# Performance work log

Hardware: AMD Instinct MI355X
Metric: run time of the kernel (lower is better)

Reference implementation:

```python
import jax, jax.numpy as jnp
import numpy as np

B, C, L = 32, 512, 4096
H, K = 8, 3            # heads, kernel_size
D = C // H             # head dim
G = 32                 # GroupNorm groups
PAD = (K - 1) // 2
EPS = 1e-5
NEG = -1e30


def setup_inputs() -> dict:
    key = jax.random.key(0)
    ks = jax.random.split(key, 7)
    s = 0.02
    return {
        "x": jax.random.normal(ks[0], (B, C, L), dtype=jnp.float32),
        "gamma": jnp.ones((C,), dtype=jnp.float32),
        "beta": jnp.zeros((C,), dtype=jnp.float32),
        "W_k": jax.random.normal(ks[1], (C, H * D), dtype=jnp.float32) * s,
        "W_v": jax.random.normal(ks[2], (C, H * D), dtype=jnp.float32) * s,
        "W_o": jax.random.normal(ks[3], (H * D, C), dtype=jnp.float32) * s,
        "q": jax.random.normal(ks[4], (H, D), dtype=jnp.float32) * s,     # learned queries (QnA)
        "rpe": jax.random.normal(ks[5], (H, K), dtype=jnp.float32) * s,   # relative-position bias
    }


def _group_norm(x, gamma, beta):
    # x: (B, C, L); normalize over (C//G, L) within each of G groups
    b, c, l = x.shape
    xg = x.reshape(b, G, (c // G) * l)
    mu = jnp.mean(xg, axis=-1, keepdims=True)
    var = jnp.var(xg, axis=-1, keepdims=True)
    xn = ((xg - mu) * jax.lax.rsqrt(var + EPS)).reshape(b, c, l)
    return xn * gamma[None, :, None] + beta[None, :, None]


def reference(x, gamma, beta, W_k, W_v, W_o, q, rpe):
    h = _group_norm(x, gamma, beta)                     # (B, C, L)
    ht = jnp.transpose(h, (0, 2, 1))                    # (B, L, C)
    k = (ht @ W_k).reshape(B, L, H, D)                  # (B, L, H, D)
    v = (ht @ W_v).reshape(B, L, H, D)

    scale = 1.0 / np.sqrt(D).astype(np.float32)
    logits = jnp.einsum('blhd,hd->blh', k, q) * scale   # (B, L, H)

    # sliding windows of size K (zero-padded; -inf logits at boundaries)
    lp = jnp.pad(logits, ((0, 0), (PAD, PAD), (0, 0)), constant_values=NEG)
    lwin = jnp.stack([lp[:, j:j + L] for j in range(K)], axis=2)      # (B, L, K, H)
    lwin = lwin + jnp.transpose(rpe)[None, None]                       # rpe: (H,K)->(K,H)
    attn = jax.nn.softmax(lwin, axis=2)                                # (B, L, K, H)

    vp = jnp.pad(v, ((0, 0), (PAD, PAD), (0, 0), (0, 0)))
    vwin = jnp.stack([vp[:, j:j + L] for j in range(K)], axis=2)       # (B, L, K, H, D)
    o = jnp.einsum('blkh,blkhd->blhd', attn, vwin).reshape(B, L, H * D)

    out = (o @ W_o)                                      # (B, L, C)
    return x + jnp.transpose(out, (0, 2, 1))             # residual, (B, C, L)
```

## Files before the change

kernel.cpp:

```cpp
#include <hip/hip_runtime.h>

#define Bb 32
#define Cc 512
#define Ll 4096
#define Hh 8
#define Dd 64
#define Gg 32
#define BLt (Bb * Ll)
#define NKV 520
#define NKVPAD 640

typedef __attribute__((ext_vector_type(4))) float f32x4;
typedef __attribute__((ext_vector_type(8))) short short8;
typedef __attribute__((ext_vector_type(4))) int int4v;

union U16 { int4v v; short s[8]; };

__device__ __forceinline__ float bf2f(short s) {
    unsigned u = ((unsigned)(unsigned short)s) << 16;
    float f; __builtin_memcpy(&f, &u, 4); return f;
}
__device__ __forceinline__ short f2bf(float f) {
    unsigned u; __builtin_memcpy(&u, &f, 4);
    u = (u + 0x7FFFu + ((u >> 16) & 1u)) >> 16;
    return (short)u;
}

__device__ __forceinline__ int swz_off(int row, int inner) {
    return row * 128 + (inner ^ ((row & 7) << 4));
}

__global__ void k_prep(const float* __restrict__ Wk, const float* __restrict__ Wv,
                       const float* __restrict__ Wo, const float* __restrict__ q,
                       short* __restrict__ Wct, short* __restrict__ Wot)
{
    int bid = blockIdx.x, t = threadIdx.x;
    if (bid < NKVPAD) {
        int n = bid;
        if (n < 512) {
            for (int k = t; k < 512; k += 64)
                Wct[n * 512 + k] = f2bf(Wv[k * 512 + n]);
        } else if (n < NKV) {
            int h = n - 512;
            for (int k = t; k < 512; k += 64) {
                float acc = 0.f;
                for (int d = 0; d < 64; ++d)
                    acc += Wk[k * 512 + h * 64 + d] * q[h * 64 + d];
                Wct[n * 512 + k] = f2bf(acc * 0.125f);
            }
        } else {
            for (int k = t; k < 512; k += 64) Wct[n * 512 + k] = 0;
        }
    } else {
        int c = bid - NKVPAD;
        for (int k = t; k < 512; k += 64)
            Wot[c * 512 + k] = f2bf(Wo[k * 512 + c]);
    }
}

__global__ void k_stats(const float* __restrict__ x, float* __restrict__ stats)
{
    int bg = blockIdx.x;
    const float* p = x + (size_t)bg * 65536;
    int t = threadIdx.x;
    float s = 0.f, ss = 0.f;
    for (int i = t * 4; i < 65536; i += 1024) {
        f32x4 v = *(const f32x4*)(p + i);
        s  += v[0] + v[1] + v[2] + v[3];
        ss += v[0]*v[0] + v[1]*v[1] + v[2]*v[2] + v[3]*v[3];
    }
    for (int o = 32; o > 0; o >>= 1) { s += __shfl_down(s, o); ss += __shfl_down(ss, o); }
    __shared__ float red[8];
    int lane = t & 63, w = t >> 6;
    if (lane == 0) { red[w] = s; red[4 + w] = ss; }
    __syncthreads();
    if (t == 0) {
        float S  = red[0] + red[1] + red[2] + red[3];
        float SS = red[4] + red[5] + red[6] + red[7];
        float mean = S * (1.0f / 65536.0f);
        float var  = SS * (1.0f / 65536.0f) - mean * mean;
        stats[bg * 2]     = mean;
        stats[bg * 2 + 1] = rsqrtf(var + 1e-5f);
    }
}

__global__ void k_norm_t(const float* __restrict__ x, const float* __restrict__ gamma,
                         const float* __restrict__ beta, const float* __restrict__ stats,
                         short* __restrict__ hT)
{
    __shared__ float tile[64 * 65];
    int b = blockIdx.z, c0 = blockIdx.y * 64, l0 = blockIdx.x * 64;
    int t = threadIdx.x;
    int lq = t & 15, cq = t >> 4;
    #pragma unroll
    for (int p = 0; p < 4; ++p) {
        int cl = cq + p * 16;
        int c = c0 + cl;
        float mean = stats[(b * 32 + (c >> 4)) * 2];
        float rstd = stats[(b * 32 + (c >> 4)) * 2 + 1];
        float a  = rstd * gamma[c];
        float bb = beta[c] - mean * a;
        f32x4 v = *(const f32x4*)(x + ((size_t)b << 21) + ((size_t)c << 12) + l0 + lq * 4);
        #pragma unroll
        for (int j = 0; j < 4; ++j) tile[cl * 65 + lq * 4 + j] = v[j] * a + bb;
    }
    __syncthreads();
    int ll = t >> 2, cq4 = t & 3;
    int bl = b * Ll + l0 + ll;
    short hbuf[16];
    #pragma unroll
    for (int j = 0; j < 16; ++j) hbuf[j] = f2bf(tile[(cq4 * 16 + j) * 65 + ll]);
    short8* dst = (short8*)(hT + (size_t)bl * 512 + c0 + cq4 * 16);
    dst[0] = *(short8*)&hbuf[0];
    dst[1] = *(short8*)&hbuf[8];
}

__launch_bounds__(256, 2)
__global__ void k_gemm1(const short* __restrict__ hT, const short* __restrict__ Wct,
                        short* __restrict__ kv)
{
    __shared__ short sA[2][8192];
    __shared__ short sB[2][8192];
    const int t = threadIdx.x;
    const int m0 = blockIdx.y * 128;
    const int n0 = blockIdx.x * 128;
    const int lane = t & 63, wid = t >> 6;
    const int wm = wid >> 1, wn = wid & 1;
    const int g = lane >> 4, ln = lane & 15;
    const int sr = t >> 1, ksh = t & 1;

    const short* gA = hT  + (size_t)(m0 + sr) * 512 + ksh * 32;
    const short* gB = Wct + (size_t)(n0 + sr) * 512 + ksh * 32;

    f32x4 acc[4][4] = {};
    U16 ra[4], rb[4];

    auto load_tile = [&](int kt) {
        #pragma unroll
        for (int q = 0; q < 4; ++q) {
            ra[q].v = *(const int4v*)(gA + kt * 64 + q * 8);
            rb[q].v = *(const int4v*)(gB + kt * 64 + q * 8);
        }
    };
    auto write_tile = [&](int buf) {
        #pragma unroll
        for (int f = 0; f < 4; ++f) {
            U16 wa, wb;
            #pragma unroll
            for (int j = 0; j < 4; ++j) {
                wa.s[j]     = ra[f >> 1].s[(f & 1) * 4 + j];
                wa.s[4 + j] = ra[2 + (f >> 1)].s[(f & 1) * 4 + j];
                wb.s[j]     = rb[f >> 1].s[(f & 1) * 4 + j];
                wb.s[4 + j] = rb[2 + (f >> 1)].s[(f & 1) * 4 + j];
            }
            int off = swz_off(sr, ksh * 64 + f * 16);
            *(int4v*)((char*)&sA[buf][0] + off) = wa.v;
            *(int4v*)((char*)&sB[buf][0] + off) = wb.v;
        }
    };
    auto compute = [&](int buf) {
        #pragma unroll
        for (int ks = 0; ks < 2; ++ks) {
            short8 af[4], bfr[4];
            #pragma unroll
            for (int i = 0; i < 4; ++i) {
                af[i]  = *(const short8*)((const char*)&sA[buf][0] + swz_off(wm * 64 + i * 16 + ln, ks * 64 + g * 16));
                bfr[i] = *(const short8*)((const char*)&sB[buf][0] + swz_off(wn * 64 + i * 16 + ln, ks * 64 + g * 16));
            }
            #pragma unroll
            for (int mi = 0; mi < 4; ++mi)
                #pragma unroll
                for (int ni = 0; ni < 4; ++ni)
                    acc[mi][ni] = __builtin_amdgcn_mfma_f32_16x16x32_bf16(af[mi], bfr[ni], acc[mi][ni], 0, 0, 0);
        }
    };

    load_tile(0); write_tile(0); __syncthreads();
    #pragma unroll 1
    for (int kt = 0; kt < 8; ++kt) {
        if (kt < 7) load_tile(kt + 1);
        compute(kt & 1);
        if (kt < 7) write_tile((kt + 1) & 1);
        __syncthreads();
    }

    #pragma unroll
    for (int mi = 0; mi < 4; ++mi)
        #pragma unroll
        for (int ni = 0; ni < 4; ++ni)
            #pragma unroll
            for (int i = 0; i < 4; ++i) {
                int m = m0 + wm * 64 + mi * 16 + g * 4 + i;
                int n = n0 + wn * 64 + ni * 16 + ln;
                if (n < NKV) kv[(size_t)m * NKV + n] = f2bf(acc[mi][ni][i]);
            }
}

__global__ void k_attnw(const short* __restrict__ kv, const float* __restrict__ rpe,
                        float* __restrict__ attnW)
{
    int tid = blockIdx.x * 256 + threadIdx.x;
    int bl = tid >> 3, h = tid & 7;
    int l = bl & (Ll - 1);
    float lg[3];
    #pragma unroll
    for (int j = 0; j < 3; ++j) {
        bool valid = (j == 1) || (j == 0 && l > 0) || (j == 2 && l < Ll - 1);
        lg[j] = valid ? (bf2f(kv[(size_t)(bl + j - 1) * NKV + 512 + h]) + rpe[h * 3 + j])
                      : -1e30f;
    }
    float m = fmaxf(lg[0], fmaxf(lg[1], lg[2]));
    float e0 = __expf(lg[0] - m), e1 = __expf(lg[1] - m), e2 = __expf(lg[2] - m);
    float inv = 1.0f / (e0 + e1 + e2);
    f32x4 w = { e0 * inv, e1 * inv, e2 * inv, 0.0f };
    *(f32x4*)(attnW + (size_t)bl * 32 + h * 4) = w;
}

__launch_bounds__(256, 2)
__global__ void k_gemm2(const short* __restrict__ Wot, const short* __restrict__ kv,
                        const float* __restrict__ attnW, const float* __restrict__ x,
                        float* __restrict__ out)
{
    __shared__ short sA[2][8192];
    __shared__ short sB[2][8192];
    const int t = threadIdx.x;
    const int m0 = blockIdx.x * 128;
    const int n0 = blockIdx.y * 128;
    const int lane = t & 63, wid = t >> 6;
    const int wm = wid >> 1, wn = wid & 1;
    const int g = lane >> 4, ln = lane & 15;
    const int sr = t >> 1, ksh = t & 1;

    const short* gA = Wot + (size_t)(m0 + sr) * 512 + ksh * 32;
    const int nrow = n0 + sr;
    const int lpos = nrow & (Ll - 1);
    const int nm1 = (lpos == 0) ? nrow : nrow - 1;
    const int np1 = (lpos == Ll - 1) ? nrow : nrow + 1;
    const short* gV0 = kv + (size_t)nrow * NKV + ksh * 32;
    const short* gVm = kv + (size_t)nm1  * NKV + ksh * 32;
    const short* gVp = kv + (size_t)np1  * NKV + ksh * 32;
    const float* gW = attnW + (size_t)nrow * 32;

    f32x4 acc[4][4] = {};
    U16 ra[4], rbm[4], rb0[4], rbp[4];
    f32x4 wv;

    auto load_tile = [&](int kt) {
        #pragma unroll
        for (int q = 0; q < 4; ++q) {
            ra[q].v  = *(const int4v*)(gA  + kt * 64 + q * 8);
            rbm[q].v = *(const int4v*)(gVm + kt * 64 + q * 8);
            rb0[q].v = *(const int4v*)(gV0 + kt * 64 + q * 8);
            rbp[q].v = *(const int4v*)(gVp + kt * 64 + q * 8);
        }
        wv = *(const f32x4*)(gW + kt * 4);
    };
    auto write_tile = [&](int buf) {
        short ob[32];
        #pragma unroll
        for (int q = 0; q < 4; ++q)
            #pragma unroll
            for (int j = 0; j < 8; ++j) {
                float o = wv[0] * bf2f(rbm[q].s[j]) + wv[1] * bf2f(rb0[q].s[j])
                        + wv[2] * bf2f(rbp[q].s[j]);
                ob[q * 8 + j] = f2bf(o);
            }
        #pragma unroll
        for (int f = 0; f < 4; ++f) {
            U16 wa, wb;
            #pragma unroll
            for (int j = 0; j < 4; ++j) {
                wa.s[j]     = ra[f >> 1].s[(f & 1) * 4 + j];
                wa.s[4 + j] = ra[2 + (f >> 1)].s[(f & 1) * 4 + j];
                wb.s[j]     = ob[4 * f + j];
                wb.s[4 + j] = ob[16 + 4 * f + j];
            }
            int off = swz_off(sr, ksh * 64 + f * 16);
            *(int4v*)((char*)&sA[buf][0] + off) = wa.v;
            *(int4v*)((char*)&sB[buf][0] + off) = wb.v;
        }
    };
    auto compute = [&](int buf) {
        #pragma unroll
        for (int ks = 0; ks < 2; ++ks) {
            short8 af[4], bfr[4];
            #pragma unroll
            for (int i = 0; i < 4; ++i) {
                af[i]  = *(const short8*)((const char*)&sA[buf][0] + swz_off(wm * 64 + i * 16 + ln, ks * 64 + g * 16));
                bfr[i] = *(const short8*)((const char*)&sB[buf][0] + swz_off(wn * 64 + i * 16 + ln, ks * 64 + g * 16));
            }
            #pragma unroll
            for (int mi = 0; mi < 4; ++mi)
                #pragma unroll
                for (int ni = 0; ni < 4; ++ni)
                    acc[mi][ni] = __builtin_amdgcn_mfma_f32_16x16x32_bf16(af[mi], bfr[ni], acc[mi][ni], 0, 0, 0);
        }
    };

    load_tile(0); write_tile(0); __syncthreads();
    #pragma unroll 1
    for (int kt = 0; kt < 8; ++kt) {
        if (kt < 7) load_tile(kt + 1);
        compute(kt & 1);
        if (kt < 7) write_tile((kt + 1) & 1);
        __syncthreads();
    }

    #pragma unroll
    for (int mi = 0; mi < 4; ++mi)
        #pragma unroll
        for (int ni = 0; ni < 4; ++ni)
            #pragma unroll
            for (int i = 0; i < 4; ++i) {
                int c = m0 + wm * 64 + mi * 16 + g * 4 + i;
                int ng = n0 + wn * 64 + ni * 16 + ln;
                int b = ng >> 12, l = ng & (Ll - 1);
                size_t off = ((size_t)b << 21) | ((size_t)c << 12) | (size_t)l;
                out[off] = x[off] + acc[mi][ni][i];
            }
}

extern "C" void kernel_launch(void* const* d_in, const int* in_sizes, int n_in,
                              void* d_out, int out_size, void* d_ws, size_t ws_size,
                              hipStream_t stream)
{
    const float* x     = (const float*)d_in[0];
    const float* gamma = (const float*)d_in[1];
    const float* beta  = (const float*)d_in[2];
    const float* Wk    = (const float*)d_in[3];
    const float* Wv    = (const float*)d_in[4];
    const float* Wo    = (const float*)d_in[5];
    const float* q     = (const float*)d_in[6];
    const float* rpe   = (const float*)d_in[7];
    float* out = (float*)d_out;

    char* ws = (char*)d_ws;
    short* Wct   = (short*)(ws + 0);
    short* Wot   = (short*)(ws + 655360);
    float* stats = (float*)(ws + 1179648);
    float* attnW = (float*)(ws + 1187840);
    short* kv    = (short*)(ws + 17965056);
    short* hT    = (short*)d_out;

    k_prep<<<1152, 64, 0, stream>>>(Wk, Wv, Wo, q, Wct, Wot);
    k_stats<<<1024, 256, 0, stream>>>(x, stats);
    k_norm_t<<<dim3(64, 8, 32), 256, 0, stream>>>(x, gamma, beta, stats, hT);
    k_gemm1<<<dim3(5, 1024), 256, 0, stream>>>(hT, Wct, kv);
    k_attnw<<<4096, 256, 0, stream>>>(kv, rpe, attnW);
    k_gemm2<<<dim3(4, 1024), 256, 0, stream>>>(Wot, kv, attnW, x, out);
}
```

Measured before the change: 612.3 us.

## Pack K-dim layout for direct global-to-LDS loads and split window combine

Weights and the normalized activations are now written in a K-permuted packed layout. This lets both GEMMs stage tiles with global_load_lds straight into swizzled LDS, instead of going through registers and doing a shuffle-and-store. V and the logits go to separate buffers. A new k_combine kernel computes the softmax window weights and the mixed output once into an intermediate buffer, and a plain GEMM then consumes it with the residual add. The aim is to cut register staging and VGPR pressure in the GEMMs and remove the 3x neighbor V reads inside gemm2. The cost is an extra ~128MB intermediate write and read, and a much larger workspace requirement, with a fallback to the old path when the workspace is too small.

```diff
diff --git a/kernel.cpp b/kernel.cpp
--- a/kernel.cpp
+++ b/kernel.cpp
@@ -12,6 +12,7 @@
 
 typedef __attribute__((ext_vector_type(4))) float f32x4;
 typedef __attribute__((ext_vector_type(8))) short short8;
+typedef __attribute__((ext_vector_type(4))) short s16x4;
 typedef __attribute__((ext_vector_type(4))) int int4v;
 
 union U16 { int4v v; short s[8]; };
@@ -26,35 +27,46 @@
     return (short)u;
 }
 
+__device__ __forceinline__ int kpack(int k) {
+    int blk = k >> 5, r = k & 31;
+    return blk * 32 + ((r & 15) >> 2) * 8 + ((r >> 4) << 2) + (r & 3);
+}
+
 __device__ __forceinline__ int swz_off(int row, int inner) {
     return row * 128 + (inner ^ ((row & 7) << 4));
 }
 
+__device__ __forceinline__ void gload16(const short* g, short* l) {
+    __builtin_amdgcn_global_load_lds((const __attribute__((address_space(1))) unsigned int*)g,
+                                     (__attribute__((address_space(3))) unsigned int*)l,
+                                     16, 0, 0);
+}
+
 __global__ void k_prep(const float* __restrict__ Wk, const float* __restrict__ Wv,
                        const float* __restrict__ Wo, const float* __restrict__ q,
-                       short* __restrict__ Wct, short* __restrict__ Wot)
+                       short* __restrict__ Wct, short* __restrict__ Wot, int packWo)
 {
     int bid = blockIdx.x, t = threadIdx.x;
     if (bid < NKVPAD) {
         int n = bid;
         if (n < 512) {
             for (int k = t; k < 512; k += 64)
-                Wct[n * 512 + k] = f2bf(Wv[k * 512 + n]);
+                Wct[n * 512 + kpack(k)] = f2bf(Wv[k * 512 + n]);
         } else if (n < NKV) {
             int h = n - 512;
             for (int k = t; k < 512; k += 64) {
                 float acc = 0.f;
                 for (int d = 0; d < 64; ++d)
                     acc += Wk[k * 512 + h * 64 + d] * q[h * 64 + d];
-                Wct[n * 512 + k] = f2bf(acc * 0.125f);
+                Wct[n * 512 + kpack(k)] = f2bf(acc * 0.125f);
             }
         } else {
-            for (int k = t; k < 512; k += 64) Wct[n * 512 + k] = 0;
+            for (int k = t; k < 512; k += 64) Wct[n * 512 + kpack(k)] = 0;
         }
     } else {
         int c = bid - NKVPAD;
         for (int k = t; k < 512; k += 64)
-            Wot[c * 512 + k] = f2bf(Wo[k * 512 + c]);
+            Wot[c * 512 + (packWo ? kpack(k) : k)] = f2bf(Wo[k * 512 + c]);
     }
 }
 
@@ -110,14 +122,18 @@
     short hbuf[16];
     #pragma unroll
     for (int j = 0; j < 16; ++j) hbuf[j] = f2bf(tile[(cq4 * 16 + j) * 65 + ll]);
-    short8* dst = (short8*)(hT + (size_t)bl * 512 + c0 + cq4 * 16);
-    dst[0] = *(short8*)&hbuf[0];
-    dst[1] = *(short8*)&hbuf[8];
-}
-
+    short* dst = hT + (size_t)bl * 512 + ((c0 >> 5) + (cq4 >> 1)) * 32 + ((cq4 & 1) << 2);
+    #pragma unroll
+    for (int jj = 0; jj < 4; ++jj) {
+        s16x4 v4 = { hbuf[jj*4+0], hbuf[jj*4+1], hbuf[jj*4+2], hbuf[jj*4+3] };
+        *(s16x4*)(dst + jj * 8) = v4;
+    }
+}
+
+template<bool PACKED>
 __launch_bounds__(256, 2)
-__global__ void k_gemm1(const short* __restrict__ hT, const short* __restrict__ Wct,
-                        short* __restrict__ kv)
+__global__ void k_gemm1(const short* __restrict__ A, const short* __restrict__ Bw,
+                        short* __restrict__ vbuf, short* __restrict__ lbuf)
 {
     __shared__ short sA[2][8192];
     __shared__ short sB[2][8192];
@@ -127,35 +143,19 @@
     const int lane = t & 63, wid = t >> 6;
     const int wm = wid >> 1, wn = wid & 1;
     const int g = lane >> 4, ln = lane & 15;
-    const int sr = t >> 1, ksh = t & 1;
-
-    const short* gA = hT  + (size_t)(m0 + sr) * 512 + ksh * 32;
-    const short* gB = Wct + (size_t)(n0 + sr) * 512 + ksh * 32;
+
+    const int srow = wid * 8 + (lane >> 3);
+    const int sinner = (((lane & 7) ^ ((lane >> 3) & 7)) << 3);
+    const short* gAs = A  + (size_t)(m0 + srow) * 512 + sinner;
+    const short* gBs = Bw + (size_t)(n0 + srow) * 512 + sinner;
 
     f32x4 acc[4][4] = {};
-    U16 ra[4], rb[4];
-
-    auto load_tile = [&](int kt) {
-        #pragma unroll
-        for (int q = 0; q < 4; ++q) {
-            ra[q].v = *(const int4v*)(gA + kt * 64 + q * 8);
-            rb[q].v = *(const int4v*)(gB + kt * 64 + q * 8);
-        }
-    };
-    auto write_tile = [&](int buf) {
-        #pragma unroll
-        for (int f = 0; f < 4; ++f) {
-            U16 wa, wb;
-            #pragma unroll
-            for (int j = 0; j < 4; ++j) {
-                wa.s[j]     = ra[f >> 1].s[(f & 1) * 4 + j];
-                wa.s[4 + j] = ra[2 + (f >> 1)].s[(f & 1) * 4 + j];
-                wb.s[j]     = rb[f >> 1].s[(f & 1) * 4 + j];
-                wb.s[4 + j] = rb[2 + (f >> 1)].s[(f & 1) * 4 + j];
-            }
-            int off = swz_off(sr, ksh * 64 + f * 16);
-            *(int4v*)((char*)&sA[buf][0] + off) = wa.v;
-            *(int4v*)((char*)&sB[buf][0] + off) = wb.v;
+
+    auto stage = [&](int kt, int buf) {
+        #pragma unroll
+        for (int gq = 0; gq < 4; ++gq) {
+            gload16(gAs + (size_t)gq * 32 * 512 + kt * 64, &sA[buf][gq * 2048 + wid * 512]);
+            gload16(gBs + (size_t)gq * 32 * 512 + kt * 64, &sB[buf][gq * 2048 + wid * 512]);
         }
     };
     auto compute = [&](int buf) {
@@ -175,24 +175,132 @@
         }
     };
 
-    load_tile(0); write_tile(0); __syncthreads();
+    stage(0, 0);
+    __syncthreads();
     #pragma unroll 1
     for (int kt = 0; kt < 8; ++kt) {
-        if (kt < 7) load_tile(kt + 1);
+        if (kt < 7) stage(kt + 1, (kt + 1) & 1);
         compute(kt & 1);
-        if (kt < 7) write_tile((kt + 1) & 1);
         __syncthreads();
     }
 
     #pragma unroll
     for (int mi = 0; mi < 4; ++mi)
         #pragma unroll
+        for (int ni = 0; ni < 4; ++ni) {
+            int n = n0 + wn * 64 + ni * 16 + ln;
+            #pragma unroll
+            for (int i = 0; i < 4; ++i) {
+                int m = m0 + wm * 64 + mi * 16 + g * 4 + i;
+                short val = f2bf(acc[mi][ni][i]);
+                if constexpr (PACKED) {
+                    if (n < 512)      vbuf[(size_t)m * 512 + kpack(n)] = val;
+                    else if (n < NKV) lbuf[(size_t)m * 8 + (n - 512)] = val;
+                } else {
+                    if (n < NKV) vbuf[(size_t)m * NKV + n] = val;
+                }
+            }
+        }
+}
+
+__global__ void k_combine(const short* __restrict__ vbuf, const short* __restrict__ lbuf,
+                          const float* __restrict__ rpe, short* __restrict__ obuf)
+{
+    int t = threadIdx.x;
+    int bl = blockIdx.x * 16 + (t >> 4);
+    int blkd = t & 15;
+    int h = blkd >> 1;
+    int l = bl & (Ll - 1);
+    int bm = (l == 0) ? bl : bl - 1;
+    int bp = (l == Ll - 1) ? bl : bl + 1;
+    float lg0 = (l > 0)      ? bf2f(lbuf[(size_t)bm * 8 + h]) + rpe[h * 3 + 0] : -1e30f;
+    float lg1 =                bf2f(lbuf[(size_t)bl * 8 + h]) + rpe[h * 3 + 1];
+    float lg2 = (l < Ll - 1) ? bf2f(lbuf[(size_t)bp * 8 + h]) + rpe[h * 3 + 2] : -1e30f;
+    float m = fmaxf(lg1, fmaxf(lg0, lg2));
+    float e0 = (l > 0)      ? __expf(lg0 - m) : 0.f;
+    float e1 =                __expf(lg1 - m);
+    float e2 = (l < Ll - 1) ? __expf(lg2 - m) : 0.f;
+    float inv = 1.0f / (e0 + e1 + e2);
+    float w0 = e0 * inv, w1 = e1 * inv, w2 = e2 * inv;
+
+    const short8* vm = (const short8*)(vbuf + (size_t)bm * 512 + blkd * 32);
+    const short8* v0 = (const short8*)(vbuf + (size_t)bl * 512 + blkd * 32);
+    const short8* vp = (const short8*)(vbuf + (size_t)bp * 512 + blkd * 32);
+    short8* dst = (short8*)(obuf + (size_t)bl * 512 + blkd * 32);
+    #pragma unroll
+    for (int qq = 0; qq < 4; ++qq) {
+        short8 a = vm[qq], b = v0[qq], c = vp[qq], r;
+        #pragma unroll
+        for (int j = 0; j < 8; ++j)
+            r[j] = f2bf(w0 * bf2f(a[j]) + w1 * bf2f(b[j]) + w2 * bf2f(c[j]));
+        dst[qq] = r;
+    }
+}
+
+__launch_bounds__(256, 2)
+__global__ void k_gemm2p(const short* __restrict__ Wot, const short* __restrict__ obuf,
+                         const float* __restrict__ x, float* __restrict__ out)
+{
+    __shared__ short sA[2][8192];
+    __shared__ short sB[2][8192];
+    const int t = threadIdx.x;
+    const int m0 = blockIdx.x * 128;
+    const int n0 = blockIdx.y * 128;
+    const int lane = t & 63, wid = t >> 6;
+    const int wm = wid >> 1, wn = wid & 1;
+    const int g = lane >> 4, ln = lane & 15;
+
+    const int srow = wid * 8 + (lane >> 3);
+    const int sinner = (((lane & 7) ^ ((lane >> 3) & 7)) << 3);
+    const short* gAs = Wot  + (size_t)(m0 + srow) * 512 + sinner;
+    const short* gBs = obuf + (size_t)(n0 + srow) * 512 + sinner;
+
+    f32x4 acc[4][4] = {};
+
+    auto stage = [&](int kt, int buf) {
+        #pragma unroll
+        for (int gq = 0; gq < 4; ++gq) {
+            gload16(gAs + (size_t)gq * 32 * 512 + kt * 64, &sA[buf][gq * 2048 + wid * 512]);
+            gload16(gBs + (size_t)gq * 32 * 512 + kt * 64, &sB[buf][gq * 2048 + wid * 512]);
+        }
+    };
+    auto compute = [&](int buf) {
+        #pragma unroll
+        for (int ks = 0; ks < 2; ++ks) {
+            short8 af[4], bfr[4];
+            #pragma unroll
+            for (int i = 0; i < 4; ++i) {
+                af[i]  = *(const short8*)((const char*)&sA[buf][0] + swz_off(wm * 64 + i * 16 + ln, ks * 64 + g * 16));
+                bfr[i] = *(const short8*)((const char*)&sB[buf][0] + swz_off(wn * 64 + i * 16 + ln, ks * 64 + g * 16));
+            }
+            #pragma unroll
+            for (int mi = 0; mi < 4; ++mi)
+                #pragma unroll
+                for (int ni = 0; ni < 4; ++ni)
+                    acc[mi][ni] = __builtin_amdgcn_mfma_f32_16x16x32_bf16(af[mi], bfr[ni], acc[mi][ni], 0, 0, 0);
+        }
+    };
+
+    stage(0, 0);
+    __syncthreads();
+    #pragma unroll 1
+    for (int kt = 0; kt < 8; ++kt) {
+        if (kt < 7) stage(kt + 1, (kt + 1) & 1);
+        compute(kt & 1);
+        __syncthreads();
+    }
+
+    #pragma unroll
+    for (int mi = 0; mi < 4; ++mi)
+        #pragma unroll
         for (int ni = 0; ni < 4; ++ni)
             #pragma unroll
             for (int i = 0; i < 4; ++i) {
-                int m = m0 + wm * 64 + mi * 16 + g * 4 + i;
-                int n = n0 + wn * 64 + ni * 16 + ln;
-                if (n < NKV) kv[(size_t)m * NKV + n] = f2bf(acc[mi][ni][i]);
+                int c = m0 + wm * 64 + mi * 16 + g * 4 + i;
+                int ng = n0 + wn * 64 + ni * 16 + ln;
+                int b = ng >> 12, l = ng & (Ll - 1);
+                size_t off = ((size_t)b << 21) | ((size_t)c << 12) | (size_t)l;
+                out[off] = x[off] + acc[mi][ni][i];
             }
 }
 
@@ -217,9 +325,9 @@
 }
 
 __launch_bounds__(256, 2)
-__global__ void k_gemm2(const short* __restrict__ Wot, const short* __restrict__ kv,
-                        const float* __restrict__ attnW, const float* __restrict__ x,
-                        float* __restrict__ out)
+__global__ void k_gemm2_fused(const short* __restrict__ Wot, const short* __restrict__ kv,
+                              const float* __restrict__ attnW, const float* __restrict__ x,
+                              float* __restrict__ out)
 {
     __shared__ short sA[2][8192];
     __shared__ short sB[2][8192];
@@ -247,23 +355,23 @@
 
     auto load_tile = [&](int kt) {
         #pragma unroll
-        for (int q = 0; q < 4; ++q) {
-            ra[q].v  = *(const int4v*)(gA  + kt * 64 + q * 8);
-            rbm[q].v = *(const int4v*)(gVm + kt * 64 + q * 8);
-            rb0[q].v = *(const int4v*)(gV0 + kt * 64 + q * 8);
-            rbp[q].v = *(const int4v*)(gVp + kt * 64 + q * 8);
+        for (int qq = 0; qq < 4; ++qq) {
+            ra[qq].v  = *(const int4v*)(gA  + kt * 64 + qq * 8);
+            rbm[qq].v = *(const int4v*)(gVm + kt * 64 + qq * 8);
+            rb0[qq].v = *(const int4v*)(gV0 + kt * 64 + qq * 8);
+            rbp[qq].v = *(const int4v*)(gVp + kt * 64 + qq * 8);
         }
         wv = *(const f32x4*)(gW + kt * 4);
     };
     auto write_tile = [&](int buf) {
         short ob[32];
         #pragma unroll
-        for (int q = 0; q < 4; ++q)
+        for (int qq = 0; qq < 4; ++qq)
             #pragma unroll
             for (int j = 0; j < 8; ++j) {
-                float o = wv[0] * bf2f(rbm[q].s[j]) + wv[1] * bf2f(rb0[q].s[j])
-                        + wv[2] * bf2f(rbp[q].s[j]);
-                ob[q * 8 + j] = f2bf(o);
+                float o = wv[0] * bf2f(rbm[qq].s[j]) + wv[1] * bf2f(rb0[qq].s[j])
+                        + wv[2] * bf2f(rbp[qq].s[j]);
+                ob[qq * 8 + j] = f2bf(o);
             }
         #pragma unroll
         for (int f = 0; f < 4; ++f) {
@@ -333,19 +441,39 @@
     const float* q     = (const float*)d_in[6];
     const float* rpe   = (const float*)d_in[7];
     float* out = (float*)d_out;
-
     char* ws = (char*)d_ws;
-    short* Wct   = (short*)(ws + 0);
-    short* Wot   = (short*)(ws + 655360);
-    float* stats = (float*)(ws + 1179648);
-    float* attnW = (float*)(ws + 1187840);
-    short* kv    = (short*)(ws + 17965056);
-    short* hT    = (short*)d_out;
-
-    k_prep<<<1152, 64, 0, stream>>>(Wk, Wv, Wo, q, Wct, Wot);
-    k_stats<<<1024, 256, 0, stream>>>(x, stats);
-    k_norm_t<<<dim3(64, 8, 32), 256, 0, stream>>>(x, gamma, beta, stats, hT);
-    k_gemm1<<<dim3(5, 1024), 256, 0, stream>>>(hT, Wct, kv);
-    k_attnw<<<4096, 256, 0, stream>>>(kv, rpe, attnW);
-    k_gemm2<<<dim3(4, 1024), 256, 0, stream>>>(Wot, kv, attnW, x, out);
-}
+
+    const size_t MB128 = 134217728ull;
+    const size_t MAIN_WS = MB128 * 2 + 655360 + 524288 + 2097152 + 8192;
+
+    if (ws_size >= MAIN_WS) {
+        short* obuf  = (short*)(ws);
+        short* vbuf  = (short*)(ws + MB128);
+        short* Wct   = (short*)(ws + 2 * MB128);
+        short* Wot   = (short*)(ws + 2 * MB128 + 655360);
+        short* lbuf  = (short*)(ws + 2 * MB128 + 655360 + 524288);
+        float* stats = (float*)(ws + 2 * MB128 + 655360 + 524288 + 2097152);
+        short* hT    = (short*)d_out;
+
+        k_prep<<<1152, 64, 0, stream>>>(Wk, Wv, Wo, q, Wct, Wot, 1);
+        k_stats<<<1024, 256, 0, stream>>>(x, stats);
+        k_norm_t<<<dim3(64, 8, 32), 256, 0, stream>>>(x, gamma, beta, stats, hT);
+        k_gemm1<true><<<dim3(5, 1024), 256, 0, stream>>>(hT, Wct, vbuf, lbuf);
+        k_combine<<<8192, 256, 0, stream>>>(vbuf, lbuf, rpe, obuf);
+        k_gemm2p<<<dim3(4, 1024), 256, 0, stream>>>(Wot, obuf, x, out);
+    } else {
+        short* Wct   = (short*)(ws + 0);
+        short* Wot   = (short*)(ws + 655360);
+        float* stats = (float*)(ws + 1179648);
+        float* attnW = (float*)(ws + 1187840);
+        short* kv    = (short*)(ws + 17965056);
+        short* hT    = (short*)d_out;
+
+        k_prep<<<1152, 64, 0, stream>>>(Wk, Wv, Wo, q, Wct, Wot, 0);
+        k_stats<<<1024, 256, 0, stream>>>(x, stats);
+        k_norm_t<<<dim3(64, 8, 32), 256, 0, stream>>>(x, gamma, beta, stats, hT);
+        k_gemm1<false><<<dim3(5, 1024), 256, 0, stream>>>(hT, Wct, kv, nullptr);
+        k_attnw<<<4096, 256, 0, stream>>>(kv, rpe, attnW);
+        k_gemm2_fused<<<dim3(4, 1024), 256, 0, stream>>>(Wot, kv, attnW, x, out);
+    }
+}
```

Measured after the change: 575.1 us. 1.06x faster.
